# Kernel optimization log

Measured on AMD Instinct MI355X. Metric: run time of the kernel, lower is better.

The kernel has to match this reference:

```python
import jax, jax.numpy as jnp
import numpy as np

N_NODES, N_EDGES, N_GRAPHS = 20000, 640000, 16
D_NODE = D_EDGE = D_GLOBAL = 64
IN_DIM, LATENT, OUT_DIM = 256, 128, 64


def setup_inputs() -> dict:
    key = jax.random.key(0)
    ks = jax.random.split(key, 12)
    node_attr = jax.random.normal(ks[0], (N_NODES, D_NODE), dtype=jnp.float32)
    edge_attr = jax.random.normal(ks[1], (N_EDGES, D_EDGE), dtype=jnp.float32)
    global_attr = jax.random.normal(ks[2], (N_GRAPHS, D_GLOBAL), dtype=jnp.float32)
    node_mask = jax.random.uniform(ks[3], (N_NODES,), dtype=jnp.float32)
    edge_mask = jax.random.uniform(ks[4], (N_EDGES,), dtype=jnp.float32)
    edge_index = jax.random.randint(ks[5], (2, N_EDGES), 0, N_NODES, dtype=jnp.int64)
    eg_index = jax.random.randint(ks[6], (N_EDGES,), 0, N_GRAPHS, dtype=jnp.int64)
    # MLP params: Linear(IN_DIM, LATENT) -> ReLU -> Linear(LATENT, OUT_DIM)
    s1 = 1.0 / np.sqrt(IN_DIM)
    s2 = 1.0 / np.sqrt(LATENT)
    W1 = jax.random.uniform(ks[7], (IN_DIM, LATENT), minval=-s1, maxval=s1, dtype=jnp.float32)
    b1 = jax.random.uniform(ks[8], (LATENT,), minval=-s1, maxval=s1, dtype=jnp.float32)
    W2 = jax.random.uniform(ks[9], (LATENT, OUT_DIM), minval=-s2, maxval=s2, dtype=jnp.float32)
    b2 = jax.random.uniform(ks[10], (OUT_DIM,), minval=-s2, maxval=s2, dtype=jnp.float32)
    return {"node_attr": node_attr, "edge_attr": edge_attr, "global_attr": global_attr,
            "node_mask": node_mask, "edge_mask": edge_mask,
            "edge_index": edge_index, "eg_index": eg_index,
            "W1": W1, "b1": b1, "W2": W2, "b2": b2}


def reference(node_attr, edge_attr, global_attr, node_mask, edge_mask,
              edge_index, eg_index, W1, b1, W2, b2):
    senders, receivers = edge_index[0], edge_index[1]
    masked_nodes = node_attr * node_mask[:, None]          # [N, d_n]
    senders_attr = masked_nodes[senders]                   # [E, d_n] gather
    receivers_attr = masked_nodes[receivers]               # [E, d_n] gather
    globals_exp = global_attr[eg_index]                    # [E, d_g] gather
    collected = jnp.concatenate(
        [edge_attr, senders_attr, receivers_attr, globals_exp], axis=-1)  # [E, IN_DIM]
    h = jax.nn.relu(collected @ W1 + b1)                   # [E, LATENT]
    out = h @ W2 + b2                                      # [E, OUT_DIM]
    return edge_mask[:, None] * out
```

## Files before the change

### kernel.cpp

```cpp
#include <hip/hip_runtime.h>
#include <stdint.h>

typedef __attribute__((ext_vector_type(8))) short short8;
typedef __attribute__((ext_vector_type(4))) float floatx4;
typedef unsigned short ushort_t;

#define E_TOTAL 640000
#define N_NODES 20000
#define M_BLK   128
#define XS_LD   264
#define HS_LD   136

__device__ __forceinline__ unsigned short f2h(float f){
    _Float16 h = (_Float16)f;
    union { _Float16 h; unsigned short u; } v; v.h = h; return v.u;
}
__device__ __forceinline__ unsigned pk2h(float a, float b){
    return (unsigned)f2h(a) | ((unsigned)f2h(b) << 16);
}

__global__ void repack_w(const float* __restrict__ W1,
                         const float* __restrict__ W2,
                         ushort_t* __restrict__ W1p,
                         ushort_t* __restrict__ W2p){
    int tid = blockIdx.x * 256 + threadIdx.x;
    if (tid < 8*8*64){
        int kt = tid >> 9, nt = (tid >> 6) & 7, l = tid & 63;
        int q = l >> 4, c = l & 15;
        ushort_t tmp[8];
        #pragma unroll
        for (int j = 0; j < 8; j++)
            tmp[j] = f2h(W1[(kt*32 + q*8 + j)*128 + nt*16 + c]);
        #pragma unroll
        for (int j = 0; j < 8; j++) W1p[tid*8 + j] = tmp[j];
    } else if (tid < 8*8*64 + 4*4*64){
        int t = tid - 8*8*64;
        int kt = t >> 8, nt = (t >> 6) & 3, l = t & 63;
        int q = l >> 4, c = l & 15;
        ushort_t tmp[8];
        #pragma unroll
        for (int j = 0; j < 8; j++)
            tmp[j] = f2h(W2[(kt*32 + q*8 + j)*64 + nt*16 + c]);
        #pragma unroll
        for (int j = 0; j < 8; j++) W2p[t*8 + j] = tmp[j];
    }
}

__global__ __launch_bounds__(256, 2)
void edge_mlp(const float* __restrict__ node_attr,
              const float* __restrict__ edge_attr,
              const float* __restrict__ global_attr,
              const float* __restrict__ node_mask,
              const float* __restrict__ edge_mask,
              const int*   __restrict__ edge_index,
              const int*   __restrict__ eg_index,
              const float* __restrict__ b1,
              const float* __restrict__ b2,
              const ushort_t* __restrict__ W1p,
              const ushort_t* __restrict__ W2p,
              float*       __restrict__ out){
    __shared__ ushort_t Xs[M_BLK * XS_LD];
    __shared__ int sidx[M_BLK], ridx[M_BLK], gidx[M_BLK];
    __shared__ float ems[M_BLK];
    ushort_t* Hs = Xs;

    const int tid = threadIdx.x;
    const int e0  = blockIdx.x * M_BLK;

    if (tid < M_BLK){
        sidx[tid] = edge_index[e0 + tid];
        ridx[tid] = edge_index[E_TOTAL + e0 + tid];
        gidx[tid] = eg_index[e0 + tid];
        ems[tid]  = edge_mask[e0 + tid];
    }
    {
        const float4* src = (const float4*)(edge_attr + (size_t)e0 * 64);
        #pragma unroll
        for (int k = 0; k < 8; k++){
            int idx = tid + k*256;
            int r = idx >> 4, c = idx & 15;
            float4 v = src[idx];
            uint2 o; o.x = pk2h(v.x, v.y); o.y = pk2h(v.z, v.w);
            *(uint2*)&Xs[r*XS_LD + c*4] = o;
        }
    }
    __syncthreads();
    {
        #pragma unroll
        for (int k = 0; k < 8; k++){
            int idx = tid + k*256; int r = idx >> 4, c = idx & 15;
            const float4* src = (const float4*)(global_attr + (size_t)gidx[r] * 64);
            float4 v = src[c];
            uint2 o; o.x = pk2h(v.x, v.y); o.y = pk2h(v.z, v.w);
            *(uint2*)&Xs[r*XS_LD + 192 + c*4] = o;
        }
    }
    {
        int r = tid >> 1, s = tid & 1;
        int idx = s ? ridx[r] : sidx[r];
        float m = node_mask[idx];
        const float4* src = (const float4*)(node_attr + (size_t)idx * 64);
        ushort_t* dst = &Xs[r*XS_LD + 64 + s*64];
        #pragma unroll
        for (int c2 = 0; c2 < 8; c2++){
            float4 a = src[2*c2], b = src[2*c2+1];
            uint4 o;
            o.x = pk2h(a.x*m, a.y*m); o.y = pk2h(a.z*m, a.w*m);
            o.z = pk2h(b.x*m, b.y*m); o.w = pk2h(b.z*m, b.w*m);
            *(uint4*)(dst + c2*8) = o;
        }
    }
    __syncthreads();

    const int w  = tid >> 6, lane = tid & 63;
    const int q  = lane >> 4, cc = lane & 15;
    const int mt0 = (w >> 1) * 4;
    const int nt0 = (w & 1) * 4;

    floatx4 acc[4][4];
    #pragma unroll
    for (int i = 0; i < 4; i++)
        #pragma unroll
        for (int j = 0; j < 4; j++) acc[i][j] = (floatx4){0.f,0.f,0.f,0.f};

    const short8* W1v = (const short8*)W1p;
    #pragma unroll
    for (int kt = 0; kt < 8; kt++){
        short8 b[4];
        #pragma unroll
        for (int j = 0; j < 4; j++) b[j] = W1v[(kt*8 + nt0 + j)*64 + lane];
        #pragma unroll
        for (int i = 0; i < 4; i++){
            const short8 a = *(const short8*)&Xs[((mt0 + i)*16 + cc)*XS_LD + kt*32 + q*8];
            #pragma unroll
            for (int j = 0; j < 4; j++)
                acc[i][j] = __builtin_amdgcn_mfma_f32_16x16x32_f16(a, b[j], acc[i][j], 0, 0, 0);
        }
    }
    __syncthreads();

    #pragma unroll
    for (int j = 0; j < 4; j++){
        int col = (nt0 + j)*16 + cc;
        float bb = b1[col];
        #pragma unroll
        for (int i = 0; i < 4; i++){
            int rowb = (mt0 + i)*16 + q*4;
            #pragma unroll
            for (int r = 0; r < 4; r++){
                float v = acc[i][j][r] + bb;
                v = v > 0.f ? v : 0.f;
                Hs[(rowb + r)*HS_LD + col] = f2h(v);
            }
        }
    }
    __syncthreads();

    floatx4 acc2[2][4];
    #pragma unroll
    for (int i = 0; i < 2; i++)
        #pragma unroll
        for (int j = 0; j < 4; j++) acc2[i][j] = (floatx4){0.f,0.f,0.f,0.f};

    const short8* W2v = (const short8*)W2p;
    #pragma unroll
    for (int kt = 0; kt < 4; kt++){
        short8 b[4];
        #pragma unroll
        for (int j = 0; j < 4; j++) b[j] = W2v[(kt*4 + j)*64 + lane];
        #pragma unroll
        for (int i = 0; i < 2; i++){
            const short8 a = *(const short8*)&Hs[((2*w + i)*16 + cc)*HS_LD + kt*32 + q*8];
            #pragma unroll
            for (int j = 0; j < 4; j++)
                acc2[i][j] = __builtin_amdgcn_mfma_f32_16x16x32_f16(a, b[j], acc2[i][j], 0, 0, 0);
        }
    }

    float bb2[4];
    #pragma unroll
    for (int j = 0; j < 4; j++) bb2[j] = b2[j*16 + cc];
    #pragma unroll
    for (int i = 0; i < 2; i++){
        #pragma unroll
        for (int r = 0; r < 4; r++){
            int row = (2*w + i)*16 + q*4 + r;
            float em = ems[row];
            size_t base = (size_t)(e0 + row) * 64;
            #pragma unroll
            for (int j = 0; j < 4; j++){
                float v = (acc2[i][j][r] + bb2[j]) * em;
                out[base + j*16 + cc] = v;
            }
        }
    }
}

extern "C" void kernel_launch(void* const* d_in, const int* in_sizes, int n_in,
                              void* d_out, int out_size, void* d_ws, size_t ws_size,
                              hipStream_t stream){
    const float* node_attr   = (const float*)d_in[0];
    const float* edge_attr   = (const float*)d_in[1];
    const float* global_attr = (const float*)d_in[2];
    const float* node_mask   = (const float*)d_in[3];
    const float* edge_mask   = (const float*)d_in[4];
    const int*   edge_index  = (const int*)d_in[5];
    const int*   eg_index    = (const int*)d_in[6];
    const float* W1          = (const float*)d_in[7];
    const float* b1          = (const float*)d_in[8];
    const float* W2          = (const float*)d_in[9];
    const float* b2          = (const float*)d_in[10];

    ushort_t* W1p = (ushort_t*)d_ws;
    ushort_t* W2p = W1p + 8*8*64*8;

    repack_w<<<20, 256, 0, stream>>>(W1, W2, W1p, W2p);
    edge_mlp<<<E_TOTAL / M_BLK, 256, 0, stream>>>(
        node_attr, edge_attr, global_attr, node_mask, edge_mask,
        edge_index, eg_index, b1, b2, W1p, W2p, (float*)d_out);
}
```

Before: 386.5 us.

## Double threads per block and drop shared index staging in edge MLP

Raises the block size from 256 to 512 threads with 4 blocks per CU requested, splitting each wave's MFMA tile in half (4x2 instead of 4x4 for GEMM1, 2x2 instead of 2x4 for GEMM2). Index, group and mask values are now read straight from global memory rather than staged in shared arrays, which removes one barrier. The node gather is split across four threads per edge. The aim is more waves in flight to hide gather latency, with fewer registers per thread. The cost is more redundant global index loads and a smaller MFMA tile per wave, so each B fragment is reused less.

```diff
diff --git a/kernel.cpp b/kernel.cpp
--- a/kernel.cpp
+++ b/kernel.cpp
@@ -6,7 +6,6 @@
 typedef unsigned short ushort_t;
 
 #define E_TOTAL 640000
-#define N_NODES 20000
 #define M_BLK   128
 #define XS_LD   264
 #define HS_LD   136
@@ -46,7 +45,7 @@
     }
 }
 
-__global__ __launch_bounds__(256, 2)
+__global__ __launch_bounds__(512, 4)
 void edge_mlp(const float* __restrict__ node_attr,
               const float* __restrict__ edge_attr,
               const float* __restrict__ global_attr,
@@ -60,87 +59,77 @@
               const ushort_t* __restrict__ W2p,
               float*       __restrict__ out){
     __shared__ ushort_t Xs[M_BLK * XS_LD];
-    __shared__ int sidx[M_BLK], ridx[M_BLK], gidx[M_BLK];
-    __shared__ float ems[M_BLK];
     ushort_t* Hs = Xs;
 
     const int tid = threadIdx.x;
     const int e0  = blockIdx.x * M_BLK;
 
-    if (tid < M_BLK){
-        sidx[tid] = edge_index[e0 + tid];
-        ridx[tid] = edge_index[E_TOTAL + e0 + tid];
-        gidx[tid] = eg_index[e0 + tid];
-        ems[tid]  = edge_mask[e0 + tid];
-    }
     {
         const float4* src = (const float4*)(edge_attr + (size_t)e0 * 64);
         #pragma unroll
-        for (int k = 0; k < 8; k++){
-            int idx = tid + k*256;
+        for (int k = 0; k < 4; k++){
+            int idx = tid + k*512;
             int r = idx >> 4, c = idx & 15;
             float4 v = src[idx];
             uint2 o; o.x = pk2h(v.x, v.y); o.y = pk2h(v.z, v.w);
             *(uint2*)&Xs[r*XS_LD + c*4] = o;
         }
     }
-    __syncthreads();
     {
         #pragma unroll
-        for (int k = 0; k < 8; k++){
-            int idx = tid + k*256; int r = idx >> 4, c = idx & 15;
-            const float4* src = (const float4*)(global_attr + (size_t)gidx[r] * 64);
+        for (int k = 0; k < 4; k++){
+            int idx = tid + k*512; int r = idx >> 4, c = idx & 15;
+            int g = eg_index[e0 + r];
+            const float4* src = (const float4*)(global_attr + (size_t)g * 64);
             float4 v = src[c];
             uint2 o; o.x = pk2h(v.x, v.y); o.y = pk2h(v.z, v.w);
             *(uint2*)&Xs[r*XS_LD + 192 + c*4] = o;
         }
     }
     {
-        int r = tid >> 1, s = tid & 1;
-        int idx = s ? ridx[r] : sidx[r];
+        int r = tid >> 2, seg = (tid >> 1) & 1, half = tid & 1;
+        int idx = edge_index[seg*E_TOTAL + e0 + r];
         float m = node_mask[idx];
-        const float4* src = (const float4*)(node_attr + (size_t)idx * 64);
-        ushort_t* dst = &Xs[r*XS_LD + 64 + s*64];
+        const float4* src = (const float4*)(node_attr + (size_t)idx * 64) + half*8;
+        ushort_t* dst = &Xs[r*XS_LD + 64 + seg*64 + half*32];
         #pragma unroll
         for (int c2 = 0; c2 < 8; c2++){
-            float4 a = src[2*c2], b = src[2*c2+1];
-            uint4 o;
-            o.x = pk2h(a.x*m, a.y*m); o.y = pk2h(a.z*m, a.w*m);
-            o.z = pk2h(b.x*m, b.y*m); o.w = pk2h(b.z*m, b.w*m);
-            *(uint4*)(dst + c2*8) = o;
+            float4 v = src[c2];
+            uint2 o; o.x = pk2h(v.x*m, v.y*m); o.y = pk2h(v.z*m, v.w*m);
+            *(uint2*)(dst + c2*4) = o;
         }
     }
     __syncthreads();
 
     const int w  = tid >> 6, lane = tid & 63;
     const int q  = lane >> 4, cc = lane & 15;
-    const int mt0 = (w >> 1) * 4;
-    const int nt0 = (w & 1) * 4;
-
-    floatx4 acc[4][4];
+    const int mt0 = (w >> 2) * 4;
+    const int nt0 = (w & 3) * 2;
+
+    floatx4 acc[4][2];
     #pragma unroll
     for (int i = 0; i < 4; i++)
         #pragma unroll
-        for (int j = 0; j < 4; j++) acc[i][j] = (floatx4){0.f,0.f,0.f,0.f};
+        for (int j = 0; j < 2; j++) acc[i][j] = (floatx4){0.f,0.f,0.f,0.f};
 
     const short8* W1v = (const short8*)W1p;
     #pragma unroll
     for (int kt = 0; kt < 8; kt++){
-        short8 b[4];
-        #pragma unroll
-        for (int j = 0; j < 4; j++) b[j] = W1v[(kt*8 + nt0 + j)*64 + lane];
+        short8 b[2];
+        #pragma unroll
+        for (int j = 0; j < 2; j++) b[j] = W1v[(kt*8 + nt0 + j)*64 + lane];
         #pragma unroll
         for (int i = 0; i < 4; i++){
             const short8 a = *(const short8*)&Xs[((mt0 + i)*16 + cc)*XS_LD + kt*32 + q*8];
             #pragma unroll
-            for (int j = 0; j < 4; j++)
+            for (int j = 0; j < 2; j++)
                 acc[i][j] = __builtin_amdgcn_mfma_f32_16x16x32_f16(a, b[j], acc[i][j], 0, 0, 0);
         }
     }
     __syncthreads();
 
     #pragma unroll
-    for (int j = 0; j < 4; j++){
+    for (int j = 0; j < 2; j++){
         int col = (nt0 + j)*16 + cc;
         float bb = b1[col];
         #pragma unroll
@@ -156,41 +145,44 @@
     }
     __syncthreads();
 
-    floatx4 acc2[2][4];
+    const int mt20 = (w >> 1) * 2;
+    const int nt20 = (w & 1) * 2;
+
+    floatx4 acc2[2][2];
     #pragma unroll
     for (int i = 0; i < 2; i++)
         #pragma unroll
-        for (int j = 0; j < 4; j++) acc2[i][j] = (floatx4){0.f,0.f,0.f,0.f};
+        for (int j = 0; j < 2; j++) acc2[i][j] = (floatx4){0.f,0.f,0.f,0.f};
 
     const short8* W2v = (const short8*)W2p;
     #pragma unroll
     for (int kt = 0; kt < 4; kt++){
-        short8 b[4];
-        #pragma unroll
-        for (int j = 0; j < 4; j++) b[j] = W2v[(kt*4 + j)*64 + lane];
+        short8 b[2];
+        #pragma unroll
+        for (int j = 0; j < 2; j++) b[j] = W2v[(kt*4 + nt20 + j)*64 + lane];
         #pragma unroll
         for (int i = 0; i < 2; i++){
-            const short8 a = *(const short8*)&Hs[((2*w + i)*16 + cc)*HS_LD + kt*32 + q*8];
-            #pragma unroll
-            for (int j = 0; j < 4; j++)
+            const short8 a = *(const short8*)&Hs[((mt20 + i)*16 + cc)*HS_LD + kt*32 + q*8];
+            #pragma unroll
+            for (int j = 0; j < 2; j++)
                 acc2[i][j] = __builtin_amdgcn_mfma_f32_16x16x32_f16(a, b[j], acc2[i][j], 0, 0, 0);
         }
     }
 
-    float bb2[4];
-    #pragma unroll
-    for (int j = 0; j < 4; j++) bb2[j] = b2[j*16 + cc];
+    float bb2[2];
+    #pragma unroll
+    for (int j = 0; j < 2; j++) bb2[j] = b2[(nt20 + j)*16 + cc];
     #pragma unroll
     for (int i = 0; i < 2; i++){
         #pragma unroll
         for (int r = 0; r < 4; r++){
-            int row = (2*w + i)*16 + q*4 + r;
-            float em = ems[row];
+            int row = (mt20 + i)*16 + q*4 + r;
+            float em = edge_mask[e0 + row];
             size_t base = (size_t)(e0 + row) * 64;
             #pragma unroll
-            for (int j = 0; j < 4; j++){
+            for (int j = 0; j < 2; j++){
                 float v = (acc2[i][j][r] + bb2[j]) * em;
-                out[base + j*16 + cc] = v;
+                out[base + (nt20 + j)*16 + cc] = v;
             }
         }
     }
@@ -215,7 +207,7 @@
     ushort_t* W2p = W1p + 8*8*64*8;
 
     repack_w<<<20, 256, 0, stream>>>(W1, W2, W1p, W2p);
-    edge_mlp<<<E_TOTAL / M_BLK, 256, 0, stream>>>(
+    edge_mlp<<<E_TOTAL / M_BLK, 512, 0, stream>>>(
         node_attr, edge_attr, global_attr, node_mask, edge_mask,
         edge_index, eg_index, b1, b2, W1p, W2p, (float*)d_out);
 }
```

Result: no change. 380.7 us (-1.5%).
